# Optimization experiments

Measured on AMD Instinct MI355X. Metric: run time of the kernel, lower is better.

The kernel has to match this reference:

```python
import jax, jax.numpy as jnp
import numpy as np

D_MODEL = 512
NHEAD = 8
HEAD_DIM = D_MODEL // NHEAD
SEQ = 4096
BATCH = 2
BASE = 10000.0


def rope_cache(seq_len, dim):
    inv_freq = 1.0 / (BASE ** (jnp.arange(0, dim, 2, dtype=jnp.float32) / dim))
    t = jnp.arange(seq_len, dtype=jnp.float32)
    freqs = jnp.einsum('i,j->ij', t, inv_freq)          # [S, dim/2]
    emb = jnp.concatenate([freqs, freqs], axis=-1)       # [S, dim]
    return jnp.cos(emb), jnp.sin(emb)


def rotate_half(x):
    h = x.shape[-1] // 2
    return jnp.concatenate([-x[..., h:], x[..., :h]], axis=-1)


def setup_inputs() -> dict:
    key = jax.random.key(0)
    ks = jax.random.split(key, 9)
    s = 1.0 / np.sqrt(D_MODEL)
    x = jax.random.normal(ks[0], (BATCH, SEQ, D_MODEL), dtype=jnp.float32)
    Wq = jax.random.uniform(ks[1], (D_MODEL, D_MODEL), jnp.float32, -s, s)
    bq = jax.random.uniform(ks[2], (D_MODEL,), jnp.float32, -s, s)
    Wk = jax.random.uniform(ks[3], (D_MODEL, D_MODEL), jnp.float32, -s, s)
    bk = jax.random.uniform(ks[4], (D_MODEL,), jnp.float32, -s, s)
    Wv = jax.random.uniform(ks[5], (D_MODEL, D_MODEL), jnp.float32, -s, s)
    bv = jax.random.uniform(ks[6], (D_MODEL,), jnp.float32, -s, s)
    Wo = jax.random.uniform(ks[7], (D_MODEL, D_MODEL), jnp.float32, -s, s)
    bo = jax.random.uniform(ks[8], (D_MODEL,), jnp.float32, -s, s)
    # causal mask: True where attention is disallowed (j > i)
    mask = jnp.triu(jnp.ones((SEQ, SEQ), dtype=bool), k=1)
    return {"x": x, "mask": mask, "Wq": Wq, "bq": bq, "Wk": Wk, "bk": bk,
            "Wv": Wv, "bv": bv, "Wo": Wo, "bo": bo}


def reference(x, mask, Wq, bq, Wk, bk, Wv, bv, Wo, bo):
    B, S, _ = x.shape
    def proj(W, b):
        y = x @ W.T + b
        return y.reshape(B, S, NHEAD, HEAD_DIM).transpose(0, 2, 1, 3)  # [B,H,S,D]
    q = proj(Wq, bq)
    k = proj(Wk, bk)
    v = proj(Wv, bv)
    cos, sin = rope_cache(S, HEAD_DIM)                    # [S, D]
    cos = cos[None, None]; sin = sin[None, None]
    q = q * cos + rotate_half(q) * sin
    k = k * cos + rotate_half(k) * sin
    scale = HEAD_DIM ** -0.5
    attn = jnp.einsum('bhid,bhjd->bhij', q, k) * scale    # [B,H,S,S]
    attn = jnp.where(mask[None, None], -jnp.inf, attn)
    attn = jax.nn.softmax(attn, axis=-1)
    out = jnp.einsum('bhij,bhjd->bhid', attn, v)          # [B,H,S,D]
    out = out.transpose(0, 2, 1, 3).reshape(B, S, D_MODEL)
    return out @ Wo.T + bo
```

## Files before the change

kernel.cpp:

```cpp
#include <hip/hip_runtime.h>
#include <hip/hip_bf16.h>

#define SEQLEN 4096
#define DMODEL 512
#define NHEADS 8

typedef short short8 __attribute__((ext_vector_type(8)));
typedef float f32x4  __attribute__((ext_vector_type(4)));
typedef float f32x16 __attribute__((ext_vector_type(16)));
typedef int   int2v  __attribute__((ext_vector_type(2)));

__device__ __forceinline__ unsigned short f2bf(float f) {
    union { float f; unsigned u; } v; v.f = f;
    unsigned r = v.u + 0x7fffu + ((v.u >> 16) & 1u);
    return (unsigned short)(r >> 16);
}
__device__ __forceinline__ float exp2v(float x) {
    float r; asm("v_exp_f32 %0, %1" : "=v"(r) : "v"(x)); return r;
}
__device__ __forceinline__ unsigned cvtpk(float lo, float hi) {
    unsigned r; asm("v_cvt_pk_bf16_f32 %0, %1, %2" : "=v"(r) : "v"(lo), "v"(hi)); return r;
}
__device__ __forceinline__ int2v pl32(int a, int b) {
    return __builtin_amdgcn_permlane32_swap(a, b, false, false);
}
__device__ __forceinline__ void gload16(const void* g, void* l) {
    __builtin_amdgcn_global_load_lds(
        (const __attribute__((address_space(1))) void*)g,
        (__attribute__((address_space(3))) void*)l, 16, 0, 0);
}

__global__ __launch_bounds__(256)
void prep_kernel(const float* __restrict__ x,
                 const float* __restrict__ Wq, const float* __restrict__ Wk,
                 const float* __restrict__ Wv, const float* __restrict__ Wo,
                 unsigned short* __restrict__ xb, unsigned short* __restrict__ Wcat,
                 float* __restrict__ ct, float* __restrict__ st) {
    const int gid = blockIdx.x, tid = threadIdx.x;
    if (gid < 4096) {
        int i = gid * 1024 + tid * 4;
        float4 v = *reinterpret_cast<const float4*>(x + i);
        ushort4 o; o.x = f2bf(v.x); o.y = f2bf(v.y); o.z = f2bf(v.z); o.w = f2bf(v.w);
        *reinterpret_cast<ushort4*>(xb + i) = o;
    } else if (gid < 5120) {
        int i = (gid - 4096) * 1024 + tid * 4;
        int z = i >> 18;
        const float* W = (z == 0) ? Wq : (z == 1) ? Wk : (z == 2) ? Wv : Wo;
        int j = i & 262143;
        float4 v = *reinterpret_cast<const float4*>(W + j);
        ushort4 o; o.x = f2bf(v.x); o.y = f2bf(v.y); o.z = f2bf(v.z); o.w = f2bf(v.w);
        *reinterpret_cast<ushort4*>(Wcat + i) = o;
    } else {
        int idx = (gid - 5120) * 256 + tid;
        int s = idx >> 5, f = idx & 31;
        float inv = powf(10000.0f, -(float)f * (1.0f / 32.0f));
        float a = (float)s * inv;
        ct[idx] = cosf(a); st[idx] = sinf(a);
    }
}

template<int MODE>
__global__ __launch_bounds__(256)
void gemm_kernel(const unsigned short* __restrict__ A,
                 const unsigned short* __restrict__ W,
                 const float* __restrict__ bq,
                 const float* __restrict__ bk,
                 const float* __restrict__ bv,
                 const float* __restrict__ ctab,
                 const float* __restrict__ stab,
                 unsigned short* __restrict__ Qb,
                 unsigned short* __restrict__ Kb,
                 unsigned short* __restrict__ Vb,
                 float* __restrict__ Fout)
{
    constexpr int K = 512;
    constexpr int NT = (MODE == 0) ? 12 : 4;
    constexpr int CPX = (MODE == 0) ? 96 : 32;
    __shared__ __align__(16) unsigned short a_sh[3][128 * 32];
    __shared__ __align__(16) unsigned short b_sh[3][128 * 32];

    const int raw = blockIdx.x;
    const int bid = (raw & 7) * CPX + (raw >> 3);
    const int bm = bid / NT, bn = bid % NT;
    const int tid = threadIdx.x;
    const int w = tid >> 6, l = tid & 63;
    const int g = l >> 4, l15 = l & 15;
    const int wr = w >> 1, wc = w & 1;

    const int sr0 = tid >> 2;
    const int swzc = (tid & 3) ^ ((sr0 >> 1) & 3);
    const unsigned wbase = (unsigned)(tid & 0xC0) * 16;
    const unsigned short* arow = A + (size_t)(bm * 128 + sr0) * K + swzc * 8;
    const unsigned short* brow = W + (size_t)(bn * 128 + sr0) * K + swzc * 8;

    f32x4 acc[4][4];
    #pragma unroll
    for (int p = 0; p < 4; ++p)
        #pragma unroll
        for (int q = 0; q < 4; ++q)
            acc[p][q] = (f32x4){0.f, 0.f, 0.f, 0.f};

    auto stage = [&](int buf, int k0) {
        char* ab = (char*)a_sh[buf];
        char* bb2 = (char*)b_sh[buf];
        gload16(arow + k0,                      ab + wbase);
        gload16(arow + (size_t)64 * K + k0,     ab + 4096 + wbase);
        gload16(brow + k0,                      bb2 + wbase);
        gload16(brow + (size_t)64 * K + k0,     bb2 + 4096 + wbase);
    };

    stage(0, 0);
    stage(1, 32);
    asm volatile("s_waitcnt vmcnt(4)" ::: "memory");
    __builtin_amdgcn_s_barrier();

    int cb = 0;
    for (int ks = 0; ks < 16; ++ks) {
        int pb = cb + 2; if (pb >= 3) pb -= 3;
        stage(pb, (ks + 2 < 16) ? (ks + 2) * 32 : 480);

        const char* ab = (const char*)a_sh[cb];
        const char* bb2 = (const char*)b_sh[cb];
        short8 af[4], bf[4];
        #pragma unroll
        for (int mt = 0; mt < 4; ++mt) {
            int r = wr * 64 + mt * 16 + l15;
            int ofs = (r * 64 + g * 16) ^ (((r >> 1) & 3) << 4);
            af[mt] = *reinterpret_cast<const short8*>(ab + ofs);
        }
        #pragma unroll
        for (int nt = 0; nt < 4; ++nt) {
            int r = wc * 64 + nt * 16 + l15;
            int ofs = (r * 64 + g * 16) ^ (((r >> 1) & 3) << 4);
            bf[nt] = *reinterpret_cast<const short8*>(bb2 + ofs);
        }
        __builtin_amdgcn_s_setprio(1);
        #pragma unroll
        for (int mt = 0; mt < 4; ++mt)
            #pragma unroll
            for (int nt = 0; nt < 4; ++nt)
                acc[mt][nt] = __builtin_amdgcn_mfma_f32_16x16x32_bf16(af[mt], bf[nt], acc[mt][nt], 0, 0, 0);
        __builtin_amdgcn_s_setprio(0);

        asm volatile("s_waitcnt vmcnt(4)" ::: "memory");
        __builtin_amdgcn_s_barrier();
        cb = (cb == 2) ? 0 : cb + 1;
    }

    const int m_base = bm * 128 + wr * 64;

    if (MODE == 1) {
        const int n_base = bn * 128 + wc * 64;
        #pragma unroll
        for (int mt = 0; mt < 4; ++mt)
            for (int nt = 0; nt < 4; ++nt) {
                int n = n_base + nt * 16 + l15;
                float bb = bq[n];
                #pragma unroll
                for (int i = 0; i < 4; ++i) {
                    int m = m_base + mt * 16 + g * 4 + i;
                    Fout[(size_t)m * 512 + n] = acc[mt][nt][i] + bb;
                }
            }
    } else {
        const int z = bn >> 2;
        const int nc0 = (bn & 3) * 128 + wc * 64;
        const float* bias = (z == 0) ? bq : (z == 1) ? bk : bv;
        if (z < 2) {
            unsigned short* Y = z ? Kb : Qb;
            const float qsc = z ? 1.0f : 0.18033688011112042f;
            #pragma unroll
            for (int mt = 0; mt < 4; ++mt)
                for (int ntl = 0; ntl < 2; ++ntl) {
                    int hd0 = (ntl * 16 + l15) & 31;
                    int n0 = nc0 + ntl * 16 + l15;
                    float bb0 = bias[n0];
                    float bb1 = bias[n0 + 32];
                    #pragma unroll
                    for (int i = 0; i < 4; ++i) {
                        int m = m_base + mt * 16 + g * 4 + i;
                        int sidx = m & (SEQLEN - 1);
                        float cs = ctab[sidx * 32 + hd0];
                        float sn = stab[sidx * 32 + hd0];
                        float v0 = acc[mt][ntl][i] + bb0;
                        float v1 = acc[mt][ntl + 2][i] + bb1;
                        Y[(size_t)m * 512 + n0]      = f2bf((v0 * cs - v1 * sn) * qsc);
                        Y[(size_t)m * 512 + n0 + 32] = f2bf((v1 * cs + v0 * sn) * qsc);
                    }
                }
        } else {
            #pragma unroll
            for (int mt = 0; mt < 4; ++mt)
                for (int nt = 0; nt < 4; ++nt) {
                    int n0 = nc0 + nt * 16 + l15;
                    float bb = bias[n0];
                    #pragma unroll
                    for (int i = 0; i < 4; ++i) {
                        int m = m_base + mt * 16 + g * 4 + i;
                        Vb[(size_t)m * 512 + n0] = f2bf(acc[mt][nt][i] + bb);
                    }
                }
        }
    }
}

__global__ __launch_bounds__(256)
void vtrans_kernel(const unsigned short* __restrict__ V, unsigned short* __restrict__ Vt) {
    __shared__ __align__(16) unsigned short t_sh[64 * 64];
    const int bx = blockIdx.x;
    const int bh = bx >> 6, stile = bx & 63;
    const int b = bh >> 3, h = bh & 7;
    const int tid = threadIdx.x;
    const int s0 = stile * 64;
    #pragma unroll
    for (int it = 0; it < 2; ++it) {
        int idx = it * 256 + tid;
        int s = idx >> 3, cb = idx & 7;
        short8 v = *reinterpret_cast<const short8*>(V + (size_t)(b * 4096 + s0 + s) * 512 + h * 64 + cb * 8);
        int ofs = (s * 128 + cb * 16) ^ ((s & 7) << 4);
        *reinterpret_cast<short8*>(reinterpret_cast<char*>(t_sh) + ofs) = v;
    }
    __syncthreads();
    #pragma unroll
    for (int it = 0; it < 2; ++it) {
        int idx = it * 256 + tid;
        int d = idx >> 3, sb = idx & 7;
        union { unsigned short u[8]; short8 s8; } o;
        #pragma unroll
        for (int j = 0; j < 8; ++j) {
            int s = sb * 8 + j;
            int ofs = (s * 128 + d * 2) ^ ((s & 7) << 4);
            o.u[j] = *reinterpret_cast<const unsigned short*>(reinterpret_cast<const char*>(t_sh) + ofs);
        }
        *reinterpret_cast<short8*>(Vt + ((size_t)(bh * 64 + d)) * SEQLEN + s0 + sb * 8) = o.s8;
    }
}

template<int SPLIT>
__global__ __launch_bounds__(256)
void attn_kernel(const unsigned short* __restrict__ Qg,
                 const unsigned short* __restrict__ Kg,
                 const unsigned short* __restrict__ Vt,
                 unsigned short* __restrict__ O,
                 float* __restrict__ Opt,
                 float* __restrict__ Ml)
{
    __shared__ __align__(16) unsigned short k_sh[3][64 * 64];
    __shared__ __align__(16) unsigned short v_sh[3][64 * 64];

    const int bx = blockIdx.x;
    int bh, qb, sp;
    if (SPLIT) {
        const int qbi = bx >> 5;
        qb = 31 - qbi;
        bh = (bx & 31) >> 1;
        sp = bx & 1;
    } else {
        bh = bx & 15; qb = 31 - (bx >> 4); sp = 0;
    }
    const int t0 = SPLIT ? sp * (qb + 1) : 0;
    const int t1 = SPLIT ? t0 + qb + 1 : 2 * qb + 2;

    const int b = bh >> 3, hh = bh & 7;
    const int tid = threadIdx.x;
    const int w = tid >> 6, l = tid & 63;
    const int l31 = l & 31, h = l >> 5;

    const size_t qkbase = (size_t)b * SEQLEN * DMODEL + hh * 64;
    const unsigned short* Vrow = Vt + (size_t)bh * 64 * SEQLEN;

    const int r0 = tid >> 3, cb0 = tid & 7;
    const int scs = cb0 ^ (r0 & 7);
    const unsigned short* ksrc0 = Kg + qkbase + (size_t)r0 * DMODEL + scs * 8;
    const unsigned short* vsrc0 = Vrow + (size_t)r0 * SEQLEN + scs * 8;

    const int swz = (l31 & 7) << 4;
    const int td = 2 * qb + (w >> 1);
    const int tlimit = td + 1;
    const int qg = qb * 128 + w * 32 + l31;

    short8 qf[4];
    const unsigned short* qrow = Qg + qkbase + (size_t)qg * DMODEL;
    #pragma unroll
    for (int kk = 0; kk < 4; ++kk)
        qf[kk] = *reinterpret_cast<const short8*>(qrow + kk * 16 + h * 8);

    f32x16 oa0, oa1;
    #pragma unroll
    for (int i = 0; i < 16; ++i) { oa0[i] = 0.f; oa1[i] = 0.f; }
    float mrun = -3.0e38f, lrun = 0.f;

    auto stage = [&](int buf, int t) {
        char* kb = (char*)k_sh[buf];
        char* vb = (char*)v_sh[buf];
        const unsigned short* kp = ksrc0 + (size_t)t * 64 * DMODEL;
        const unsigned short* vp = vsrc0 + t * 64;
        gload16(kp,                     kb + tid * 16);
        gload16(kp + 32 * DMODEL,       kb + 4096 + tid * 16);
        gload16(vp,                     vb + tid * 16);
        gload16(vp + 32 * SEQLEN,       vb + 4096 + tid * 16);
    };

    int cb = t0 % 3;
    stage(cb, t0);
    {
        int nb = cb + 1; if (nb >= 3) nb -= 3;
        stage(nb, (t0 + 1 < t1) ? t0 + 1 : t1 - 1);
    }
    asm volatile("s_waitcnt vmcnt(4)" ::: "memory");
    __builtin_amdgcn_s_barrier();

    for (int t = t0; t < t1; ++t) {
        int pb = cb + 2; if (pb >= 3) pb -= 3;
        stage(pb, (t + 2 < t1) ? t + 2 : t1 - 1);

        if (t < tlimit) {
            const char* kb = (const char*)k_sh[cb];
            const char* vb = (const char*)v_sh[cb];

            f32x16 st0, st1;
            #pragma unroll
            for (int i = 0; i < 16; ++i) { st0[i] = 0.f; st1[i] = 0.f; }
            __builtin_amdgcn_s_setprio(1);
            #pragma unroll
            for (int kk = 0; kk < 4; ++kk) {
                short8 kf0 = *reinterpret_cast<const short8*>(kb + l31 * 128 + ((kk * 32 + h * 16) ^ swz));
                short8 kf1 = *reinterpret_cast<const short8*>(kb + (32 + l31) * 128 + ((kk * 32 + h * 16) ^ swz));
                st0 = __builtin_amdgcn_mfma_f32_32x32x16_bf16(kf0, qf[kk], st0, 0, 0, 0);
                st1 = __builtin_amdgcn_mfma_f32_32x32x16_bf16(kf1, qf[kk], st1, 0, 0, 0);
            }
            __builtin_amdgcn_s_setprio(0);

            if (t == td) {
                #pragma unroll
                for (int r = 0; r < 16; ++r) {
                    int rp = (r & 3) + 8 * (r >> 2) + 4 * h;
                    int kv0 = t * 64 + rp;
                    if (kv0 > qg)      st0[r] = -3.0e38f;
                    if (kv0 + 32 > qg) st1[r] = -3.0e38f;
                }
            }

            float mx[16];
            #pragma unroll
            for (int r = 0; r < 16; ++r) mx[r] = fmaxf(st0[r], st1[r]);
            #pragma unroll
            for (int str = 8; str >= 1; str >>= 1)
                #pragma unroll
                for (int r = 0; r < str; ++r) mx[r] = fmaxf(mx[r], mx[r + str]);
            int2v rp2 = pl32(__float_as_int(mx[0]), __float_as_int(mx[0]));
            float pm = fmaxf(__int_as_float(rp2[0]), __int_as_float(rp2[1]));

            float mn = mrun;
            if (__any(pm > mrun + 8.0f)) {
                mn = fmaxf(mrun, pm);
                float al = exp2v(mrun - mn);
                mrun = mn;
                lrun *= al;
                #pragma unroll
                for (int r = 0; r < 16; ++r) { oa0[r] *= al; oa1[r] *= al; }
            }
            #pragma unroll
            for (int r = 0; r < 16; ++r) st0[r] = exp2v(st0[r] - mn);
            #pragma unroll
            for (int r = 0; r < 16; ++r) st1[r] = exp2v(st1[r] - mn);
            float sm[16];
            #pragma unroll
            for (int r = 0; r < 16; ++r) sm[r] = st0[r] + st1[r];
            #pragma unroll
            for (int str = 8; str >= 1; str >>= 1)
                #pragma unroll
                for (int r = 0; r < str; ++r) sm[r] += sm[r + str];
            int2v rs2 = pl32(__float_as_int(sm[0]), __float_as_int(sm[0]));
            lrun += __int_as_float(rs2[0]) + __int_as_float(rs2[1]);

            __builtin_amdgcn_s_setprio(1);
            #pragma unroll
            for (int bb = 0; bb < 4; ++bb) {
                const int rb = (bb & 1) * 8;
                float p0, p1, p2, p3, p4, p5, p6, p7;
                if (bb < 2) {
                    p0 = st0[rb + 0]; p1 = st0[rb + 1]; p2 = st0[rb + 2]; p3 = st0[rb + 3];
                    p4 = st0[rb + 4]; p5 = st0[rb + 5]; p6 = st0[rb + 6]; p7 = st0[rb + 7];
                } else {
                    p0 = st1[rb + 0]; p1 = st1[rb + 1]; p2 = st1[rb + 2]; p3 = st1[rb + 3];
                    p4 = st1[rb + 4]; p5 = st1[rb + 5]; p6 = st1[rb + 6]; p7 = st1[rb + 7];
                }
                int pk0 = (int)cvtpk(p0, p1);
                int pk1 = (int)cvtpk(p2, p3);
                int pk2 = (int)cvtpk(p4, p5);
                int pk3 = (int)cvtpk(p6, p7);
                int2v r02 = pl32(pk0, pk2);
                int2v r13 = pl32(pk1, pk3);
                union { int u[4]; short8 s8; } pw;
                pw.u[0] = r02[0];
                pw.u[1] = r13[0];
                pw.u[2] = r02[1];
                pw.u[3] = r13[1];

                short8 vf0 = *reinterpret_cast<const short8*>(vb + l31 * 128 + ((bb * 32 + h * 16) ^ swz));
                short8 vf1 = *reinterpret_cast<const short8*>(vb + (32 + l31) * 128 + ((bb * 32 + h * 16) ^ swz));
                oa0 = __builtin_amdgcn_mfma_f32_32x32x16_bf16(vf0, pw.s8, oa0, 0, 0, 0);
                oa1 = __builtin_amdgcn_mfma_f32_32x32x16_bf16(vf1, pw.s8, oa1, 0, 0, 0);
            }
            __builtin_amdgcn_s_setprio(0);
        }

        asm volatile("s_waitcnt vmcnt(4)" ::: "memory");
        __builtin_amdgcn_s_barrier();
        cb = (cb == 2) ? 0 : cb + 1;
    }

    if (SPLIT) {
        *reinterpret_cast<float2*>(Ml + ((size_t)(sp * 16 + bh) * 4096 + qg) * 2) =
            make_float2(mrun, lrun);
        float* opbase = Opt + (size_t)(sp * 16 + bh) * 64 * 4096;
        #pragma unroll
        for (int r = 0; r < 16; r += 2) {
            int d0 = (r & 3) + 8 * (r >> 2) + 4 * h;
            opbase[(size_t)d0 * 4096 + qg]        = oa0[r];
            opbase[(size_t)(d0 + 1) * 4096 + qg]  = oa0[r + 1];
            opbase[(size_t)(d0 + 32) * 4096 + qg] = oa1[r];
            opbase[(size_t)(d0 + 33) * 4096 + qg] = oa1[r + 1];
        }
    } else {
        float inv = 1.0f / lrun;
        unsigned short* orow = O + qkbase + (size_t)qg * DMODEL;
        #pragma unroll
        for (int r = 0; r < 16; r += 2) {
            int d0 = (r & 3) + 8 * (r >> 2) + 4 * h;
            *reinterpret_cast<unsigned*>(orow + d0)      = cvtpk(oa0[r] * inv, oa0[r + 1] * inv);
            *reinterpret_cast<unsigned*>(orow + 32 + d0) = cvtpk(oa1[r] * inv, oa1[r + 1] * inv);
        }
    }
}

__global__ __launch_bounds__(256)
void combine_kernel(const float* __restrict__ Opt, const float* __restrict__ Ml,
                    unsigned short* __restrict__ O) {
    __shared__ float a0_sh[64], a1_sh[64];
    __shared__ unsigned short o_sh[64][72];
    const int bx = blockIdx.x;
    const int bh = bx >> 6, qt = bx & 63;
    const int b = bh >> 3, hh = bh & 7;
    const int q0 = qt * 64;
    const int tid = threadIdx.x;

    if (tid < 64) {
        int q = q0 + tid;
        float2 ml0 = *reinterpret_cast<const float2*>(Ml + ((size_t)bh * 4096 + q) * 2);
        float2 ml1 = *reinterpret_cast<const float2*>(Ml + ((size_t)(16 + bh) * 4096 + q) * 2);
        float m = fmaxf(ml0.x, ml1.x);
        float a0 = exp2v(ml0.x - m), a1 = exp2v(ml1.x - m);
        float inv = 1.0f / (a0 * ml0.y + a1 * ml1.y);
        a0_sh[tid] = a0 * inv;
        a1_sh[tid] = a1 * inv;
    }
    __syncthreads();

    const int d = tid >> 2, q4 = (tid & 3) * 16;
    const float* p0 = Opt + ((size_t)bh * 64 + d) * 4096 + q0 + q4;
    const float* p1 = Opt + ((size_t)(16 + bh) * 64 + d) * 4096 + q0 + q4;
    #pragma unroll
    for (int j = 0; j < 16; j += 4) {
        float4 v0 = *reinterpret_cast<const float4*>(p0 + j);
        float4 v1 = *reinterpret_cast<const float4*>(p1 + j);
        int q = q4 + j;
        o_sh[q + 0][d] = f2bf(a0_sh[q + 0] * v0.x + a1_sh[q + 0] * v1.x);
        o_sh[q + 1][d] = f2bf(a0_sh[q + 1] * v0.y + a1_sh[q + 1] * v1.y);
        o_sh[q + 2][d] = f2bf(a0_sh[q + 2] * v0.z + a1_sh[q + 2] * v1.z);
        o_sh[q + 3][d] = f2bf(a0_sh[q + 3] * v0.w + a1_sh[q + 3] * v1.w);
    }
    __syncthreads();

    const int qw = tid >> 2, dc = (tid & 3) * 16;
    unsigned short* orow = O + ((size_t)(b * 4096 + q0 + qw)) * 512 + hh * 64 + dc;
    #pragma unroll
    for (int j = 0; j < 2; ++j) {
        union { ushort4 h4[2]; short8 s8; } u;
        u.h4[0] = *reinterpret_cast<const ushort4*>(&o_sh[qw][dc + j * 8]);
        u.h4[1] = *reinterpret_cast<const ushort4*>(&o_sh[qw][dc + j * 8 + 4]);
        *reinterpret_cast<short8*>(orow + j * 8) = u.s8;
    }
}

extern "C" void kernel_launch(void* const* d_in, const int* in_sizes, int n_in,
                              void* d_out, int out_size, void* d_ws, size_t ws_size,
                              hipStream_t stream) {
    const float* x  = (const float*)d_in[0];
    const float* Wq = (const float*)d_in[2];
    const float* bq = (const float*)d_in[3];
    const float* Wk = (const float*)d_in[4];
    const float* bk = (const float*)d_in[5];
    const float* Wv = (const float*)d_in[6];
    const float* bv = (const float*)d_in[7];
    const float* Wo = (const float*)d_in[8];
    const float* bo = (const float*)d_in[9];
    float* out = (float*)d_out;

    const int MD = 8192 * 512;
    const int WD = 512 * 512;
    unsigned short* ws  = (unsigned short*)d_ws;
    unsigned short* xb  = ws;
    unsigned short* Qb  = xb + MD;
    unsigned short* Kb  = Qb + MD;
    unsigned short* Vb  = Kb + MD;
    unsigned short* Ob  = Vb + MD;
    unsigned short* Wcat = Ob + MD;
    float* ctab = (float*)(Wcat + 4 * WD);
    float* stab = ctab + SEQLEN * 32;
    unsigned short* Vt = xb;
    float* Opt = (float*)((char*)d_ws + 45088768ull);
    float* Ml  = (float*)((char*)d_ws + 78643200ull);
    const size_t NEED = 79691776ull;
    const bool split = (ws_size >= NEED);

    prep_kernel<<<5632, 256, 0, stream>>>(x, Wq, Wk, Wv, Wo, xb, Wcat, ctab, stab);

    gemm_kernel<0><<<dim3(64 * 12), 256, 0, stream>>>(
        xb, Wcat, bq, bk, bv, ctab, stab, Qb, Kb, Vb, nullptr);

    vtrans_kernel<<<1024, 256, 0, stream>>>(Vb, Vt);

    if (split) {
        attn_kernel<1><<<dim3(1024), 256, 0, stream>>>(Qb, Kb, Vt, nullptr, Opt, Ml);
        combine_kernel<<<dim3(1024), 256, 0, stream>>>(Opt, Ml, Ob);
    } else {
        attn_kernel<0><<<dim3(512), 256, 0, stream>>>(Qb, Kb, Vt, Ob, nullptr, nullptr);
    }

    gemm_kernel<1><<<dim3(64 * 4), 256, 0, stream>>>(
        Ob, Wcat + 3 * WD, bo, nullptr, nullptr, nullptr, nullptr,
        nullptr, nullptr, nullptr, out);
}
```

Measured before the change: 232.0 us.

## Fuse V transpose into QKV GEMM, double per-wave queries in attention, bf16 partials

The QKV GEMM epilogue for V tiles now transposes through shared memory and writes Vt directly, which removes the separate transpose kernel and its extra global round trip. The attention kernel now has each wave process 64 queries (two 32-row sets) against every K/V tile, so each K/V LDS load is reused twice and the grid is halved. Split-K partial outputs are stored in bf16 instead of fp32, which halves combine traffic at some cost in precision. Launch bounds on the attention kernel request 2 blocks per CU, and the larger accumulator count may raise register pressure or cause spills.

```diff
diff --git a/kernel.cpp b/kernel.cpp
--- a/kernel.cpp
+++ b/kernel.cpp
@@ -14,6 +14,9 @@
     union { float f; unsigned u; } v; v.f = f;
     unsigned r = v.u + 0x7fffu + ((v.u >> 16) & 1u);
     return (unsigned short)(r >> 16);
+}
+__device__ __forceinline__ float bf2f(unsigned short u) {
+    union { unsigned u; float f; } v; v.u = (unsigned)u << 16; return v.f;
 }
 __device__ __forceinline__ float exp2v(float x) {
     float r; asm("v_exp_f32 %0, %1" : "=v"(r) : "v"(x)); return r;
@@ -70,14 +73,13 @@
                  const float* __restrict__ stab,
                  unsigned short* __restrict__ Qb,
                  unsigned short* __restrict__ Kb,
-                 unsigned short* __restrict__ Vb,
+                 unsigned short* __restrict__ Vt,
                  float* __restrict__ Fout)
 {
     constexpr int K = 512;
     constexpr int NT = (MODE == 0) ? 12 : 4;
     constexpr int CPX = (MODE == 0) ? 96 : 32;
-    __shared__ __align__(16) unsigned short a_sh[3][128 * 32];
-    __shared__ __align__(16) unsigned short b_sh[3][128 * 32];
+    __shared__ __align__(16) unsigned short smem[3][2][128 * 32];
 
     const int raw = blockIdx.x;
     const int bid = (raw & 7) * CPX + (raw >> 3);
@@ -101,8 +103,8 @@
             acc[p][q] = (f32x4){0.f, 0.f, 0.f, 0.f};
 
     auto stage = [&](int buf, int k0) {
-        char* ab = (char*)a_sh[buf];
-        char* bb2 = (char*)b_sh[buf];
+        char* ab = (char*)smem[buf][0];
+        char* bb2 = (char*)smem[buf][1];
         gload16(arow + k0,                      ab + wbase);
         gload16(arow + (size_t)64 * K + k0,     ab + 4096 + wbase);
         gload16(brow + k0,                      bb2 + wbase);
@@ -119,8 +121,8 @@
         int pb = cb + 2; if (pb >= 3) pb -= 3;
         stage(pb, (ks + 2 < 16) ? (ks + 2) * 32 : 480);
 
-        const char* ab = (const char*)a_sh[cb];
-        const char* bb2 = (const char*)b_sh[cb];
+        const char* ab = (const char*)smem[cb][0];
+        const char* bb2 = (const char*)smem[cb][1];
         short8 af[4], bf[4];
         #pragma unroll
         for (int mt = 0; mt < 4; ++mt) {
@@ -189,77 +191,65 @@
                     }
                 }
         } else {
+            asm volatile("s_waitcnt vmcnt(0)" ::: "memory");
+            __builtin_amdgcn_s_barrier();
+            char* T = (char*)smem;
             #pragma unroll
             for (int mt = 0; mt < 4; ++mt)
+                #pragma unroll
                 for (int nt = 0; nt < 4; ++nt) {
-                    int n0 = nc0 + nt * 16 + l15;
-                    float bb = bias[n0];
+                    int nv_l = wc * 64 + nt * 16 + l15;
+                    float bb = bias[(bn & 3) * 128 + nv_l];
                     #pragma unroll
-                    for (int i = 0; i < 4; ++i) {
-                        int m = m_base + mt * 16 + g * 4 + i;
-                        Vb[(size_t)m * 512 + n0] = f2bf(acc[mt][nt][i] + bb);
+                    for (int i = 0; i < 4; i += 2) {
+                        int m_l = wr * 64 + mt * 16 + g * 4 + i;
+                        unsigned u = cvtpk(acc[mt][nt][i] + bb, acc[mt][nt][i + 1] + bb);
+                        int byte0 = nv_l * 256 + ((m_l * 2) ^ ((nv_l & 7) << 4));
+                        *reinterpret_cast<unsigned*>(T + byte0) = u;
                     }
                 }
-        }
-    }
-}
-
-__global__ __launch_bounds__(256)
-void vtrans_kernel(const unsigned short* __restrict__ V, unsigned short* __restrict__ Vt) {
-    __shared__ __align__(16) unsigned short t_sh[64 * 64];
-    const int bx = blockIdx.x;
-    const int bh = bx >> 6, stile = bx & 63;
-    const int b = bh >> 3, h = bh & 7;
-    const int tid = threadIdx.x;
-    const int s0 = stile * 64;
-    #pragma unroll
-    for (int it = 0; it < 2; ++it) {
-        int idx = it * 256 + tid;
-        int s = idx >> 3, cb = idx & 7;
-        short8 v = *reinterpret_cast<const short8*>(V + (size_t)(b * 4096 + s0 + s) * 512 + h * 64 + cb * 8);
-        int ofs = (s * 128 + cb * 16) ^ ((s & 7) << 4);
-        *reinterpret_cast<short8*>(reinterpret_cast<char*>(t_sh) + ofs) = v;
-    }
-    __syncthreads();
-    #pragma unroll
-    for (int it = 0; it < 2; ++it) {
-        int idx = it * 256 + tid;
-        int d = idx >> 3, sb = idx & 7;
-        union { unsigned short u[8]; short8 s8; } o;
-        #pragma unroll
-        for (int j = 0; j < 8; ++j) {
-            int s = sb * 8 + j;
-            int ofs = (s * 128 + d * 2) ^ ((s & 7) << 4);
-            o.u[j] = *reinterpret_cast<const unsigned short*>(reinterpret_cast<const char*>(t_sh) + ofs);
-        }
-        *reinterpret_cast<short8*>(Vt + ((size_t)(bh * 64 + d)) * SEQLEN + s0 + sb * 8) = o.s8;
+            __builtin_amdgcn_s_barrier();
+            const int b_out = bm >> 5;
+            const int s0 = (bm & 31) * 128;
+            #pragma unroll
+            for (int p = 0; p < 8; ++p) {
+                int nv_l = p * 16 + (tid >> 4);
+                int c = tid & 15;
+                int byte = nv_l * 256 + ((c * 16) ^ ((nv_l & 7) << 4));
+                short8 v = *reinterpret_cast<const short8*>(T + byte);
+                int nv_g = (bn & 3) * 128 + nv_l;
+                int hg = nv_g >> 6, d = nv_g & 63;
+                *reinterpret_cast<short8*>(
+                    Vt + ((size_t)((b_out * 8 + hg) * 64 + d)) * SEQLEN + s0 + c * 8) = v;
+            }
+        }
     }
 }
 
 template<int SPLIT>
-__global__ __launch_bounds__(256)
+__global__ __launch_bounds__(256, 2)
 void attn_kernel(const unsigned short* __restrict__ Qg,
                  const unsigned short* __restrict__ Kg,
                  const unsigned short* __restrict__ Vt,
                  unsigned short* __restrict__ O,
-                 float* __restrict__ Opt,
+                 unsigned short* __restrict__ Opt,
                  float* __restrict__ Ml)
 {
     __shared__ __align__(16) unsigned short k_sh[3][64 * 64];
     __shared__ __align__(16) unsigned short v_sh[3][64 * 64];
 
     const int bx = blockIdx.x;
-    int bh, qb, sp;
+    int bh, qsuper, sp;
     if (SPLIT) {
-        const int qbi = bx >> 5;
-        qb = 31 - qbi;
-        bh = (bx & 31) >> 1;
+        qsuper = 15 - (bx >> 5);
+        bh = (bx >> 1) & 15;
         sp = bx & 1;
     } else {
-        bh = bx & 15; qb = 31 - (bx >> 4); sp = 0;
-    }
-    const int t0 = SPLIT ? sp * (qb + 1) : 0;
-    const int t1 = SPLIT ? t0 + qb + 1 : 2 * qb + 2;
+        qsuper = 15 - (bx >> 4); bh = bx & 15; sp = 0;
+    }
+    const int HT = 2 * qsuper + 2;
+    const int t0 = SPLIT ? sp * HT : 0;
+    const int t1 = SPLIT ? t0 + HT : 2 * HT;
 
     const int b = bh >> 3, hh = bh & 7;
     const int tid = threadIdx.x;
@@ -275,30 +265,84 @@
     const unsigned short* vsrc0 = Vrow + (size_t)r0 * SEQLEN + scs * 8;
 
     const int swz = (l31 & 7) << 4;
-    const int td = 2 * qb + (w >> 1);
+    const int td = 4 * qsuper + w;
     const int tlimit = td + 1;
-    const int qg = qb * 128 + w * 32 + l31;
-
-    short8 qf[4];
-    const unsigned short* qrow = Qg + qkbase + (size_t)qg * DMODEL;
+    const int qg0 = qsuper * 256 + w * 64 + l31;
+    const int qg1 = qg0 + 32;
+
+    short8 qf0[4], qf1[4];
+    {
+        const unsigned short* qr0 = Qg + qkbase + (size_t)qg0 * DMODEL;
+        const unsigned short* qr1 = Qg + qkbase + (size_t)qg1 * DMODEL;
+        #pragma unroll
+        for (int kk = 0; kk < 4; ++kk) {
+            qf0[kk] = *reinterpret_cast<const short8*>(qr0 + kk * 16 + h * 8);
+            qf1[kk] = *reinterpret_cast<const short8*>(qr1 + kk * 16 + h * 8);
+        }
+    }
+
+    f32x16 oa00, oa01, oa10, oa11;
     #pragma unroll
-    for (int kk = 0; kk < 4; ++kk)
-        qf[kk] = *reinterpret_cast<const short8*>(qrow + kk * 16 + h * 8);
-
-    f32x16 oa0, oa1;
-    #pragma unroll
-    for (int i = 0; i < 16; ++i) { oa0[i] = 0.f; oa1[i] = 0.f; }
-    float mrun = -3.0e38f, lrun = 0.f;
+    for (int i = 0; i < 16; ++i) { oa00[i] = 0.f; oa01[i] = 0.f; oa10[i] = 0.f; oa11[i] = 0.f; }
+    float m0 = -3.0e38f, l0 = 0.f, m1 = -3.0e38f, l1 = 0.f;
 
     auto stage = [&](int buf, int t) {
         char* kb = (char*)k_sh[buf];
         char* vb = (char*)v_sh[buf];
         const unsigned short* kp = ksrc0 + (size_t)t * 64 * DMODEL;
         const unsigned short* vp = vsrc0 + t * 64;
-        gload16(kp,                     kb + tid * 16);
-        gload16(kp + 32 * DMODEL,       kb + 4096 + tid * 16);
-        gload16(vp,                     vb + tid * 16);
-        gload16(vp + 32 * SEQLEN,       vb + 4096 + tid * 16);
+        gload16(kp,                kb + tid * 16);
+        gload16(kp + 32 * DMODEL,  kb + 4096 + tid * 16);
+        gload16(vp,                vb + tid * 16);
+        gload16(vp + 32 * SEQLEN,  vb + 4096 + tid * 16);
+    };
+
+    auto softmax_set = [&](f32x16& sA, f32x16& sB, float& mr, float& lr,
+                           f32x16& oaA, f32x16& oaB, short8* pw) {
+        float mx[16];
+        #pragma unroll
+        for (int r = 0; r < 16; ++r) mx[r] = fmaxf(sA[r], sB[r]);
+        #pragma unroll
+        for (int str = 8; str >= 1; str >>= 1)
+            #pragma unroll
+            for (int r = 0; r < str; ++r) mx[r] = fmaxf(mx[r], mx[r + str]);
+        int2v rp2 = pl32(__float_as_int(mx[0]), __float_as_int(mx[0]));
+        float pm = fmaxf(__int_as_float(rp2[0]), __int_as_float(rp2[1]));
+        float mn = mr;
+        if (__any(pm > mr + 8.0f)) {
+            mn = fmaxf(mr, pm);
+            float al = exp2v(mr - mn);
+            mr = mn; lr *= al;
+            #pragma unroll
+            for (int r = 0; r < 16; ++r) { oaA[r] *= al; oaB[r] *= al; }
+        }
+        #pragma unroll
+        for (int r = 0; r < 16; ++r) sA[r] = exp2v(sA[r] - mn);
+        #pragma unroll
+        for (int r = 0; r < 16; ++r) sB[r] = exp2v(sB[r] - mn);
+        float sm[16];
+        #pragma unroll
+        for (int r = 0; r < 16; ++r) sm[r] = sA[r] + sB[r];
+        #pragma unroll
+        for (int str = 8; str >= 1; str >>= 1)
+            #pragma unroll
+            for (int r = 0; r < str; ++r) sm[r] += sm[r + str];
+        int2v rs2 = pl32(__float_as_int(sm[0]), __float_as_int(sm[0]));
+        lr += __int_as_float(rs2[0]) + __int_as_float(rs2[1]);
+        #pragma unroll
+        for (int bb = 0; bb < 4; ++bb) {
+            const int rb = (bb & 1) * 8;
+            const f32x16& s = (bb < 2) ? sA : sB;
+            int pk0 = (int)cvtpk(s[rb + 0], s[rb + 1]);
+            int pk1 = (int)cvtpk(s[rb + 2], s[rb + 3]);
+            int pk2 = (int)cvtpk(s[rb + 4], s[rb + 5]);
+            int pk3 = (int)cvtpk(s[rb + 6], s[rb + 7]);
+            int2v r02 = pl32(pk0, pk2);
+            int2v r13 = pl32(pk1, pk3);
+            union { int u[4]; short8 s8; } w_;
+            w_.u[0] = r02[0]; w_.u[1] = r13[0]; w_.u[2] = r02[1]; w_.u[3] = r13[1];
+            pw[bb] = w_.s8;
+        }
     };
 
     int cb = t0 % 3;
@@ -318,16 +362,18 @@
             const char* kb = (const char*)k_sh[cb];
             const char* vb = (const char*)v_sh[cb];
 
-            f32x16 st0, st1;
-            #pragma unroll
-            for (int i = 0; i < 16; ++i) { st0[i] = 0.f; st1[i] = 0.f; }
+            f32x16 s00, s01, s10, s11;
+            #pragma unroll
+            for (int i = 0; i < 16; ++i) { s00[i] = 0.f; s01[i] = 0.f; s10[i] = 0.f; s11[i] = 0.f; }
             __builtin_amdgcn_s_setprio(1);
             #pragma unroll
             for (int kk = 0; kk < 4; ++kk) {
                 short8 kf0 = *reinterpret_cast<const short8*>(kb + l31 * 128 + ((kk * 32 + h * 16) ^ swz));
                 short8 kf1 = *reinterpret_cast<const short8*>(kb + (32 + l31) * 128 + ((kk * 32 + h * 16) ^ swz));
-                st0 = __builtin_amdgcn_mfma_f32_32x32x16_bf16(kf0, qf[kk], st0, 0, 0, 0);
-                st1 = __builtin_amdgcn_mfma_f32_32x32x16_bf16(kf1, qf[kk], st1, 0, 0, 0);
+                s00 = __builtin_amdgcn_mfma_f32_32x32x16_bf16(kf0, qf0[kk], s00, 0, 0, 0);
+                s01 = __builtin_amdgcn_mfma_f32_32x32x16_bf16(kf1, qf0[kk], s01, 0, 0, 0);
+                s10 = __builtin_amdgcn_mfma_f32_32x32x16_bf16(kf0, qf1[kk], s10, 0, 0, 0);
+                s11 = __builtin_amdgcn_mfma_f32_32x32x16_bf16(kf1, qf1[kk], s11, 0, 0, 0);
             }
             __builtin_amdgcn_s_setprio(0);
 
@@ -336,72 +382,26 @@
                 for (int r = 0; r < 16; ++r) {
                     int rp = (r & 3) + 8 * (r >> 2) + 4 * h;
                     int kv0 = t * 64 + rp;
-                    if (kv0 > qg)      st0[r] = -3.0e38f;
-                    if (kv0 + 32 > qg) st1[r] = -3.0e38f;
+                    if (kv0 > qg0)      s00[r] = -3.0e38f;
+                    if (kv0 + 32 > qg0) s01[r] = -3.0e38f;
+                    if (kv0 > qg1)      s10[r] = -3.0e38f;
+                    if (kv0 + 32 > qg1) s11[r] = -3.0e38f;
                 }
             }
 
-            float mx[16];
-            #pragma unroll
-            for (int r = 0; r < 16; ++r) mx[r] = fmaxf(st0[r], st1[r]);
-            #pragma unroll
-            for (int str = 8; str >= 1; str >>= 1)
-                #pragma unroll
-                for (int r = 0; r < str; ++r) mx[r] = fmaxf(mx[r], mx[r + str]);
-            int2v rp2 = pl32(__float_as_int(mx[0]), __float_as_int(mx[0]));
-            float pm = fmaxf(__int_as_float(rp2[0]), __int_as_float(rp2[1]));
-
-            float mn = mrun;
-            if (__any(pm > mrun + 8.0f)) {
-                mn = fmaxf(mrun, pm);
-                float al = exp2v(mrun - mn);
-                mrun = mn;
-                lrun *= al;
-                #pragma unroll
-                for (int r = 0; r < 16; ++r) { oa0[r] *= al; oa1[r] *= al; }
-            }
-            #pragma unroll
-            for (int r = 0; r < 16; ++r) st0[r] = exp2v(st0[r] - mn);
-            #pragma unroll
-            for (int r = 0; r < 16; ++r) st1[r] = exp2v(st1[r] - mn);
-            float sm[16];
-            #pragma unroll
-            for (int r = 0; r < 16; ++r) sm[r] = st0[r] + st1[r];
-            #pragma unroll
-            for (int str = 8; str >= 1; str >>= 1)
-                #pragma unroll
-                for (int r = 0; r < str; ++r) sm[r] += sm[r + str];
-            int2v rs2 = pl32(__float_as_int(sm[0]), __float_as_int(sm[0]));
-            lrun += __int_as_float(rs2[0]) + __int_as_float(rs2[1]);
+            short8 pw0[4], pw1[4];
+            softmax_set(s00, s01, m0, l0, oa00, oa01, pw0);
+            softmax_set(s10, s11, m1, l1, oa10, oa11, pw1);
 
             __builtin_amdgcn_s_setprio(1);
             #pragma unroll
             for (int bb = 0; bb < 4; ++bb) {
-                const int rb = (bb & 1) * 8;
-                float p0, p1, p2, p3, p4, p5, p6, p7;
-                if (bb < 2) {
-                    p0 = st0[rb + 0]; p1 = st0[rb + 1]; p2 = st0[rb + 2]; p3 = st0[rb + 3];
-                    p4 = st0[rb + 4]; p5 = st0[rb + 5]; p6 = st0[rb + 6]; p7 = st0[rb + 7];
-                } else {
-                    p0 = st1[rb + 0]; p1 = st1[rb + 1]; p2 = st1[rb + 2]; p3 = st1[rb + 3];
-                    p4 = st1[rb + 4]; p5 = st1[rb + 5]; p6 = st1[rb + 6]; p7 = st1[rb + 7];
-                }
-                int pk0 = (int)cvtpk(p0, p1);
-                int pk1 = (int)cvtpk(p2, p3);
-                int pk2 = (int)cvtpk(p4, p5);
-                int pk3 = (int)cvtpk(p6, p7);
-                int2v r02 = pl32(pk0, pk2);
-                int2v r13 = pl32(pk1, pk3);
-                union { int u[4]; short8 s8; } pw;
-                pw.u[0] = r02[0];
-                pw.u[1] = r13[0];
-                pw.u[2] = r02[1];
-                pw.u[3] = r13[1];
-
                 short8 vf0 = *reinterpret_cast<const short8*>(vb + l31 * 128 + ((bb * 32 + h * 16) ^ swz));
                 short8 vf1 = *reinterpret_cast<const short8*>(vb + (32 + l31) * 128 + ((bb * 32 + h * 16) ^ swz));
-                oa0 = __builtin_amdgcn_mfma_f32_32x32x16_bf16(vf0, pw.s8, oa0, 0, 0, 0);
-                oa1 = __builtin_amdgcn_mfma_f32_32x32x16_bf16(vf1, pw.s8, oa1, 0, 0, 0);
+                oa00 = __builtin_amdgcn_mfma_f32_32x32x16_bf16(vf0, pw0[bb], oa00, 0, 0, 0);
+                oa01 = __builtin_amdgcn_mfma_f32_32x32x16_bf16(vf1, pw0[bb], oa01, 0, 0, 0);
+                oa10 = __builtin_amdgcn_mfma_f32_32x32x16_bf16(vf0, pw1[bb], oa10, 0, 0, 0);
+                oa11 = __builtin_amdgcn_mfma_f32_32x32x16_bf16(vf1, pw1[bb], oa11, 0, 0, 0);
             }
             __builtin_amdgcn_s_setprio(0);
         }
@@ -412,31 +412,44 @@
     }
 
     if (SPLIT) {
-        *reinterpret_cast<float2*>(Ml + ((size_t)(sp * 16 + bh) * 4096 + qg) * 2) =
-            make_float2(mrun, lrun);
-        float* opbase = Opt + (size_t)(sp * 16 + bh) * 64 * 4096;
+        float* mlb = Ml + (size_t)(sp * 16 + bh) * 4096 * 2;
+        *reinterpret_cast<float2*>(mlb + (size_t)qg0 * 2) = make_float2(m0, l0);
+        *reinterpret_cast<float2*>(mlb + (size_t)qg1 * 2) = make_float2(m1, l1);
+        unsigned short* opb = Opt + (size_t)(sp * 16 + bh) * 64 * 4096;
         #pragma unroll
         for (int r = 0; r < 16; r += 2) {
             int d0 = (r & 3) + 8 * (r >> 2) + 4 * h;
-            opbase[(size_t)d0 * 4096 + qg]        = oa0[r];
-            opbase[(size_t)(d0 + 1) * 4096 + qg]  = oa0[r + 1];
-            opbase[(size_t)(d0 + 32) * 4096 + qg] = oa1[r];
-            opbase[(size_t)(d0 + 33) * 4096 + qg] = oa1[r + 1];
+            unsigned u;
+            u = cvtpk(oa00[r], oa00[r + 1]);
+            opb[(size_t)d0 * 4096 + qg0] = (unsigned short)u;
+            opb[(size_t)(d0 + 1) * 4096 + qg0] = (unsigned short)(u >> 16);
+            u = cvtpk(oa01[r], oa01[r + 1]);
+            opb[(size_t)(d0 + 32) * 4096 + qg0] = (unsigned short)u;
+            opb[(size_t)(d0 + 33) * 4096 + qg0] = (unsigned short)(u >> 16);
+            u = cvtpk(oa10[r], oa10[r + 1]);
+            opb[(size_t)d0 * 4096 + qg1] = (unsigned short)u;
+            opb[(size_t)(d0 + 1) * 4096 + qg1] = (unsigned short)(u >> 16);
+            u = cvtpk(oa11[r], oa11[r + 1]);
+            opb[(size_t)(d0 + 32) * 4096 + qg1] = (unsigned short)u;
+            opb[(size_t)(d0 + 33) * 4096 + qg1] = (unsigned short)(u >> 16);
         }
     } else {
-        float inv = 1.0f / lrun;
-        unsigned short* orow = O + qkbase + (size_t)qg * DMODEL;
+        float inv0 = 1.0f / l0, inv1 = 1.0f / l1;
+        unsigned short* or0 = O + qkbase + (size_t)qg0 * DMODEL;
+        unsigned short* or1 = O + qkbase + (size_t)qg1 * DMODEL;
         #pragma unroll
         for (int r = 0; r < 16; r += 2) {
             int d0 = (r & 3) + 8 * (r >> 2) + 4 * h;
-            *reinterpret_cast<unsigned*>(orow + d0)      = cvtpk(oa0[r] * inv, oa0[r + 1] * inv);
-            *reinterpret_cast<unsigned*>(orow + 32 + d0) = cvtpk(oa1[r] * inv, oa1[r + 1] * inv);
+            *reinterpret_cast<unsigned*>(or0 + d0)      = cvtpk(oa00[r] * inv0, oa00[r + 1] * inv0);
+            *reinterpret_cast<unsigned*>(or0 + 32 + d0) = cvtpk(oa01[r] * inv0, oa01[r + 1] * inv0);
+            *reinterpret_cast<unsigned*>(or1 + d0)      = cvtpk(oa10[r] * inv1, oa10[r + 1] * inv1);
+            *reinterpret_cast<unsigned*>(or1 + 32 + d0) = cvtpk(oa11[r] * inv1, oa11[r + 1] * inv1);
         }
     }
 }
 
 __global__ __launch_bounds__(256)
-void combine_kernel(const float* __restrict__ Opt, const float* __restrict__ Ml,
+void combine_kernel(const unsigned short* __restrict__ Opt, const float* __restrict__ Ml,
                     unsigned short* __restrict__ O) {
     __shared__ float a0_sh[64], a1_sh[64];
     __shared__ unsigned short o_sh[64][72];
@@ -459,17 +472,18 @@
     __syncthreads();
 
     const int d = tid >> 2, q4 = (tid & 3) * 16;
-    const float* p0 = Opt + ((size_t)bh * 64 + d) * 4096 + q0 + q4;
-    const float* p1 = Opt + ((size_t)(16 + bh) * 64 + d) * 4096 + q0 + q4;
+    const unsigned short* p0 = Opt + ((size_t)bh * 64 + d) * 4096 + q0 + q4;
+    const unsigned short* p1 = Opt + ((size_t)(16 + bh) * 64 + d) * 4096 + q0 + q4;
     #pragma unroll
-    for (int j = 0; j < 16; j += 4) {
-        float4 v0 = *reinterpret_cast<const float4*>(p0 + j);
-        float4 v1 = *reinterpret_cast<const float4*>(p1 + j);
-        int q = q4 + j;
-        o_sh[q + 0][d] = f2bf(a0_sh[q + 0] * v0.x + a1_sh[q + 0] * v1.x);
-        o_sh[q + 1][d] = f2bf(a0_sh[q + 1] * v0.y + a1_sh[q + 1] * v1.y);
-        o_sh[q + 2][d] = f2bf(a0_sh[q + 2] * v0.z + a1_sh[q + 2] * v1.z);
-        o_sh[q + 3][d] = f2bf(a0_sh[q + 3] * v0.w + a1_sh[q + 3] * v1.w);
+    for (int j = 0; j < 16; j += 8) {
+        short8 v0 = *reinterpret_cast<const short8*>(p0 + j);
+        short8 v1 = *reinterpret_cast<const short8*>(p1 + j);
+        #pragma unroll
+        for (int e = 0; e < 8; ++e) {
+            int q = q4 + j + e;
+            o_sh[q][d] = f2bf(a0_sh[q] * bf2f((unsigned short)v0[e]) +
+                              a1_sh[q] * bf2f((unsigned short)v1[e]));
+        }
     }
     __syncthreads();
 
@@ -504,13 +518,12 @@
     unsigned short* xb  = ws;
     unsigned short* Qb  = xb + MD;
     unsigned short* Kb  = Qb + MD;
-    unsigned short* Vb  = Kb + MD;
-    unsigned short* Ob  = Vb + MD;
+    unsigned short* Vt  = Kb + MD;
+    unsigned short* Ob  = Vt + MD;
     unsigned short* Wcat = Ob + MD;
     float* ctab = (float*)(Wcat + 4 * WD);
     float* stab = ctab + SEQLEN * 32;
-    unsigned short* Vt = xb;
-    float* Opt = (float*)((char*)d_ws + 45088768ull);
+    unsigned short* Opt = (unsigned short*)((char*)d_ws + 45088768ull);
     float* Ml  = (float*)((char*)d_ws + 78643200ull);
     const size_t NEED = 79691776ull;
     const bool split = (ws_size >= NEED);
@@ -518,15 +531,13 @@
     prep_kernel<<<5632, 256, 0, stream>>>(x, Wq, Wk, Wv, Wo, xb, Wcat, ctab, stab);
 
     gemm_kernel<0><<<dim3(64 * 12), 256, 0, stream>>>(
-        xb, Wcat, bq, bk, bv, ctab, stab, Qb, Kb, Vb, nullptr);
-
-    vtrans_kernel<<<1024, 256, 0, stream>>>(Vb, Vt);
+        xb, Wcat, bq, bk, bv, ctab, stab, Qb, Kb, Vt, nullptr);
 
     if (split) {
-        attn_kernel<1><<<dim3(1024), 256, 0, stream>>>(Qb, Kb, Vt, nullptr, Opt, Ml);
+        attn_kernel<1><<<dim3(512), 256, 0, stream>>>(Qb, Kb, Vt, nullptr, Opt, Ml);
         combine_kernel<<<dim3(1024), 256, 0, stream>>>(Opt, Ml, Ob);
     } else {
-        attn_kernel<0><<<dim3(512), 256, 0, stream>>>(Qb, Kb, Vt, Ob, nullptr, nullptr);
+        attn_kernel<0><<<dim3(256), 256, 0, stream>>>(Qb, Kb, Vt, Ob, nullptr, nullptr);
     }
 
     gemm_kernel<1><<<dim3(64 * 4), 256, 0, stream>>>(
```

After: 227.0 us. 2.1% less time.
